# Optimization experiments

Hardware: AMD Instinct MI355X
Metric: run time of the kernel (lower is better)

Reference implementation:

```python
import jax, jax.numpy as jnp
import numpy as np

NUM_HEADS = 16

def setup_inputs() -> dict:
    key = jax.random.key(0)
    ks = jax.random.split(key, 5)
    N, T, D = 16, 4096, 1024
    # Linear weights stored as (in, out): y = x @ W + b (equivalent to torch x @ W.T + b)
    return {
        "x": jax.random.normal(ks[0], (N, T, D), jnp.float32),
        "w_qkv": jax.random.normal(ks[1], (D, 3 * D), jnp.float32) * (D ** -0.5),
        "b_qkv": jax.random.normal(ks[2], (3 * D,), jnp.float32) * 0.02,
        "w_proj": jax.random.normal(ks[3], (D, D), jnp.float32) * (D ** -0.5),
        "b_proj": jax.random.normal(ks[4], (D,), jnp.float32) * 0.02,
    }

def reference(x, w_qkv, b_qkv, w_proj, b_proj):
    N, T, D = x.shape
    H = NUM_HEADS
    hd = D // H
    scale = hd ** -0.5
    qkv = x @ w_qkv + b_qkv                      # (N,T,3D)
    qkv = qkv.reshape(N, T, 3, H, hd)
    q, k, v = qkv[:, :, 0], qkv[:, :, 1], qkv[:, :, 2]   # each (N,T,H,hd)
    # Faithful to source: matmul over last two dims -> scores across HEADS, (N,T,H,H)
    attn = jnp.einsum('nthd,ntgd->nthg', q * scale, k)
    attn = jax.nn.softmax(attn, axis=-1)
    out = jnp.einsum('nthg,ntgd->nthd', attn, v)         # (N,T,H,hd)
    # Faithful: transpose(2,1) then flatten -> (N,H,T,hd).reshape(N,T,D)
    out = out.transpose(0, 2, 1, 3).reshape(N, T, D)
    return out @ w_proj + b_proj
```

## Files before the change

kernel.cpp:

```cpp
#include <hip/hip_runtime.h>
#include <hip/hip_bf16.h>
#include <stdint.h>

typedef __bf16 bf16x8 __attribute__((ext_vector_type(8)));
typedef float f32x4 __attribute__((ext_vector_type(4)));
typedef unsigned short us8 __attribute__((ext_vector_type(8)));

__device__ __forceinline__ float bf2f(unsigned short u) {
    return __uint_as_float(((unsigned)u) << 16);
}
__device__ __forceinline__ unsigned short f2bf(float f) {
    __bf16 b = (__bf16)f;
    return __builtin_bit_cast(unsigned short, b);
}

__device__ __forceinline__ void gload16(const char* g, char* l) {
    __builtin_amdgcn_global_load_lds(
        (const __attribute__((address_space(1))) void*)g,
        (__attribute__((address_space(3))) void*)l, 16, 0, 0);
}

__global__ __launch_bounds__(256) void transpose_cast(
    const float* __restrict__ in, unsigned short* __restrict__ out,
    int K, int N)
{
    __shared__ float tile[32][33];
    const int tx = threadIdx.x, ty = threadIdx.y;
    const int n0 = blockIdx.x * 32, k0 = blockIdx.y * 32;
    #pragma unroll
    for (int i = 0; i < 32; i += 8)
        tile[ty + i][tx] = in[(long)(k0 + ty + i) * N + n0 + tx];
    __syncthreads();
    #pragma unroll
    for (int i = 0; i < 32; i += 8)
        out[(long)(n0 + ty + i) * K + k0 + tx] = f2bf(tile[tx][ty + i]);
}

__global__ __launch_bounds__(256) void cast_f32_bf16(
    const float* __restrict__ in, unsigned short* __restrict__ out, long n)
{
    const long stride = (long)gridDim.x * 256 * 8;
    for (long i = ((long)blockIdx.x * 256 + threadIdx.x) * 8; i < n; i += stride) {
        const f32x4 u0 = *(const f32x4*)&in[i];
        const f32x4 u1 = *(const f32x4*)&in[i + 4];
        us8 w;
        #pragma unroll
        for (int e = 0; e < 4; ++e) { w[e] = f2bf(u0[e]); w[e + 4] = f2bf(u1[e]); }
        *(us8*)&out[i] = w;
    }
}

#define MFMA16x16(a, b, c) __builtin_amdgcn_mfma_f32_16x16x32_bf16(a, b, c, 0, 0, 0)

template<bool OUT_BF16>
__global__ __launch_bounds__(512, 2)
void gemm256(const unsigned short* __restrict__ A,
             const unsigned short* __restrict__ BT,
             const float* __restrict__ bias,
             void* __restrict__ Cp,
             int M, int N, int K)
{
    extern __shared__ char smem[];
    const int tid  = threadIdx.x;
    const int lane = tid & 63;
    const int w    = tid >> 6;
    const int wm   = w >> 2;
    const int wn   = w & 3;

    const int nwg  = gridDim.x;
    const int bid0 = blockIdx.x;
    const int bid  = (bid0 & 7) * (nwg >> 3) + (bid0 >> 3);
    const int nbx  = N >> 8;
    const int bx   = bid % nbx, by = bid / nbx;
    const long rowStart = (long)by * 256;
    const int  colStart = bx * 256;

    const int  KT = K >> 6;
    const long Kb = (long)K * 2;

    const int srow = w * 8 + (lane >> 3);
    const int scol = ((lane & 7) ^ (lane >> 3)) << 4;
    const char* aStage = (const char*)A  + (rowStart + srow) * Kb + scol;
    const char* bStage = (const char*)BT + ((long)colStart + srow) * Kb + scol;
    const int ldsW = w * 1024;

    const int fr = lane & 15;
    const int kq = lane >> 4;
    const int kswz0 = (kq * 16)      ^ ((fr & 7) << 4);
    const int kswz1 = (64 + kq * 16) ^ ((fr & 7) << 4);
    const int aRowBase = (wm * 128 + fr) * 128;
    const int bRowBase = (wn * 64 + fr) * 128 + 32768;

    f32x4 acc[8][4] = {};

    #pragma unroll
    for (int tt = 0; tt < 2; ++tt) {
        #pragma unroll
        for (int j = 0; j < 4; ++j)
            gload16(aStage + (long)j * 64 * Kb + (long)tt * 128,
                    smem + tt * 65536 + j * 8192 + ldsW);
        #pragma unroll
        for (int j = 0; j < 4; ++j)
            gload16(bStage + (long)j * 64 * Kb + (long)tt * 128,
                    smem + tt * 65536 + 32768 + j * 8192 + ldsW);
    }

    #pragma unroll 2
    for (int t = 0; t < KT; ++t) {
        const int bufOff = (t & 1) * 65536;
        if (t < KT - 1) asm volatile("s_waitcnt vmcnt(8)");
        else            asm volatile("s_waitcnt vmcnt(0)");
        __builtin_amdgcn_s_barrier();
        __builtin_amdgcn_sched_barrier(0);

        bf16x8 a0[4][2], b01[2][2];
        #pragma unroll
        for (int mi = 0; mi < 4; ++mi) {
            a0[mi][0] = *(const bf16x8*)(smem + bufOff + aRowBase + mi * 2048 + kswz0);
            a0[mi][1] = *(const bf16x8*)(smem + bufOff + aRowBase + mi * 2048 + kswz1);
        }
        #pragma unroll
        for (int ni = 0; ni < 2; ++ni) {
            b01[ni][0] = *(const bf16x8*)(smem + bufOff + bRowBase + ni * 2048 + kswz0);
            b01[ni][1] = *(const bf16x8*)(smem + bufOff + bRowBase + ni * 2048 + kswz1);
        }
        __builtin_amdgcn_s_setprio(1);
        #pragma unroll
        for (int mi = 0; mi < 4; ++mi)
            #pragma unroll
            for (int ni = 0; ni < 2; ++ni) {
                acc[mi][ni] = MFMA16x16(a0[mi][0], b01[ni][0], acc[mi][ni]);
                acc[mi][ni] = MFMA16x16(a0[mi][1], b01[ni][1], acc[mi][ni]);
            }
        __builtin_amdgcn_s_setprio(0);
        __builtin_amdgcn_s_barrier();
        __builtin_amdgcn_sched_barrier(0);

        bf16x8 b23[2][2];
        #pragma unroll
        for (int nj = 0; nj < 2; ++nj) {
            b23[nj][0] = *(const bf16x8*)(smem + bufOff + bRowBase + (2 + nj) * 2048 + kswz0);
            b23[nj][1] = *(const bf16x8*)(smem + bufOff + bRowBase + (2 + nj) * 2048 + kswz1);
        }
        __builtin_amdgcn_s_setprio(1);
        #pragma unroll
        for (int mi = 0; mi < 4; ++mi)
            #pragma unroll
            for (int nj = 0; nj < 2; ++nj) {
                acc[mi][2 + nj] = MFMA16x16(a0[mi][0], b23[nj][0], acc[mi][2 + nj]);
                acc[mi][2 + nj] = MFMA16x16(a0[mi][1], b23[nj][1], acc[mi][2 + nj]);
            }
        __builtin_amdgcn_s_setprio(0);
        __builtin_amdgcn_s_barrier();
        __builtin_amdgcn_sched_barrier(0);
        if (t + 2 < KT) {
            gload16(aStage + (long)0 * 64 * Kb + (long)(t + 2) * 128,
                    smem + bufOff + 0 * 8192 + ldsW);
            gload16(aStage + (long)2 * 64 * Kb + (long)(t + 2) * 128,
                    smem + bufOff + 2 * 8192 + ldsW);
        }

        bf16x8 a4[4][2];
        #pragma unroll
        for (int mi = 0; mi < 4; ++mi) {
            a4[mi][0] = *(const bf16x8*)(smem + bufOff + aRowBase + (4 + mi) * 2048 + kswz0);
            a4[mi][1] = *(const bf16x8*)(smem + bufOff + aRowBase + (4 + mi) * 2048 + kswz1);
        }
        __builtin_amdgcn_s_setprio(1);
        #pragma unroll
        for (int mi = 0; mi < 4; ++mi)
            #pragma unroll
            for (int nj = 0; nj < 2; ++nj) {
                acc[4 + mi][2 + nj] = MFMA16x16(a4[mi][0], b23[nj][0], acc[4 + mi][2 + nj]);
                acc[4 + mi][2 + nj] = MFMA16x16(a4[mi][1], b23[nj][1], acc[4 + mi][2 + nj]);
            }
        __builtin_amdgcn_s_setprio(0);
        __builtin_amdgcn_s_barrier();
        __builtin_amdgcn_sched_barrier(0);
        if (t + 2 < KT) {
            #pragma unroll
            for (int j = 0; j < 4; ++j)
                gload16(bStage + (long)j * 64 * Kb + (long)(t + 2) * 128,
                        smem + bufOff + 32768 + j * 8192 + ldsW);
            gload16(aStage + (long)1 * 64 * Kb + (long)(t + 2) * 128,
                    smem + bufOff + 1 * 8192 + ldsW);
            gload16(aStage + (long)3 * 64 * Kb + (long)(t + 2) * 128,
                    smem + bufOff + 3 * 8192 + ldsW);
        }

        __builtin_amdgcn_s_setprio(1);
        #pragma unroll
        for (int mi = 0; mi < 4; ++mi)
            #pragma unroll
            for (int ni = 0; ni < 2; ++ni) {
                acc[4 + mi][ni] = MFMA16x16(a4[mi][0], b01[ni][0], acc[4 + mi][ni]);
                acc[4 + mi][ni] = MFMA16x16(a4[mi][1], b01[ni][1], acc[4 + mi][ni]);
            }
        __builtin_amdgcn_s_setprio(0);
        __builtin_amdgcn_sched_barrier(0);
    }

    float bv[4];
    #pragma unroll
    for (int ni = 0; ni < 4; ++ni)
        bv[ni] = bias[colStart + wn * 64 + ni * 16 + fr];
    #pragma unroll
    for (int mi = 0; mi < 8; ++mi) {
        #pragma unroll
        for (int ni = 0; ni < 4; ++ni) {
            const int col = colStart + wn * 64 + ni * 16 + fr;
            #pragma unroll
            for (int e = 0; e < 4; ++e) {
                const long row = rowStart + wm * 128 + mi * 16 + kq * 4 + e;
                const float val = acc[mi][ni][e] + bv[ni];
                if constexpr (OUT_BF16)
                    ((unsigned short*)Cp)[row * N + col] = f2bf(val);
                else
                    ((float*)Cp)[row * N + col] = val;
            }
        }
    }
}

__global__ __launch_bounds__(256) void attn_kernel(
    const unsigned short* __restrict__ qkv, unsigned short* __restrict__ out)
{
    __shared__ unsigned short qkvs[4][3072];
    __shared__ float ps[4][256];
    __shared__ unsigned short os[4][1024];
    const int tid = threadIdx.x, lane = tid & 63, wave = tid >> 6;
    const long blockTok = (long)blockIdx.x * 4;

    const unsigned short* src = qkv + blockTok * 3072;
    unsigned short* dstBase = &qkvs[0][0];
    #pragma unroll
    for (int i = 0; i < 6; ++i) {
        const int o = (i * 256 + tid) * 8;
        *(us8*)&dstBase[o] = *(const us8*)&src[o];
    }
    __syncthreads();

    const unsigned short* q = &qkvs[wave][0];
    const unsigned short* kk = &qkvs[wave][1024];
    const unsigned short* vv = &qkvs[wave][2048];
    const int h = lane >> 2, g4 = lane & 3;

    float s[4] = {0.f, 0.f, 0.f, 0.f};
    #pragma unroll
    for (int d0 = 0; d0 < 64; d0 += 8) {
        const us8 q8 = *(const us8*)&q[h * 64 + d0];
        float qf[8];
        #pragma unroll
        for (int e = 0; e < 8; ++e) qf[e] = bf2f(q8[e]);
        #pragma unroll
        for (int j = 0; j < 4; ++j) {
            const us8 k8 = *(const us8*)&kk[(g4 * 4 + j) * 64 + d0];
            #pragma unroll
            for (int e = 0; e < 8; ++e) s[j] += qf[e] * bf2f(k8[e]);
        }
    }
    #pragma unroll
    for (int j = 0; j < 4; ++j) s[j] *= 0.125f;

    float mx = fmaxf(fmaxf(s[0], s[1]), fmaxf(s[2], s[3]));
    mx = fmaxf(mx, __shfl_xor(mx, 1, 64));
    mx = fmaxf(mx, __shfl_xor(mx, 2, 64));
    float p[4], sum = 0.f;
    #pragma unroll
    for (int j = 0; j < 4; ++j) { p[j] = expf(s[j] - mx); sum += p[j]; }
    sum += __shfl_xor(sum, 1, 64);
    sum += __shfl_xor(sum, 2, 64);
    const float inv = 1.f / sum;
    #pragma unroll
    for (int j = 0; j < 4; ++j) ps[wave][h * 16 + g4 * 4 + j] = p[j] * inv;
    __syncthreads();

    const int db = lane & 3;
    float o16[16] = {};
    #pragma unroll
    for (int gq = 0; gq < 4; ++gq) {
        const f32x4 pv = *(const f32x4*)&ps[wave][h * 16 + gq * 4];
        #pragma unroll
        for (int j = 0; j < 4; ++j) {
            const float pg = pv[j];
            const int g = gq * 4 + j;
            const us8 v8a = *(const us8*)&vv[g * 64 + db * 16];
            const us8 v8b = *(const us8*)&vv[g * 64 + db * 16 + 8];
            #pragma unroll
            for (int e = 0; e < 8; ++e) {
                o16[e]     += pg * bf2f(v8a[e]);
                o16[8 + e] += pg * bf2f(v8b[e]);
            }
        }
    }
    us8 w0, w1;
    #pragma unroll
    for (int e = 0; e < 8; ++e) { w0[e] = f2bf(o16[e]); w1[e] = f2bf(o16[8 + e]); }
    *(us8*)&os[wave][h * 64 + db * 16] = w0;
    *(us8*)&os[wave][h * 64 + db * 16 + 8] = w1;
    __syncthreads();

    #pragma unroll
    for (int i = 0; i < 2; ++i) {
        const int c = i * 256 + tid;
        const int w2 = c >> 7;
        const int cc = c & 127;
        const long m = blockTok + w2;
        const long n_ = m >> 12;
        const int t = (int)(m & 4095);
        const int hh = cc >> 3, slot = cc & 7;
        const long row = n_ * 4096 + hh * 256 + (t >> 4);
        const long colb = (long)(t & 15) * 128 + slot * 16;
        *(us8*)((char*)out + row * 2048 + colb) = *(const us8*)&os[w2][cc * 8];
    }
}

extern "C" void kernel_launch(void* const* d_in, const int* in_sizes, int n_in,
                              void* d_out, int out_size, void* d_ws, size_t ws_size,
                              hipStream_t stream) {
    const float* x      = (const float*)d_in[0];
    const float* w_qkv  = (const float*)d_in[1];
    const float* b_qkv  = (const float*)d_in[2];
    const float* w_proj = (const float*)d_in[3];
    const float* b_proj = (const float*)d_in[4];

    const long M = 65536;
    const size_t QKV_B = (size_t)M * 3072 * 2;
    const size_t XB_B  = (size_t)M * 1024 * 2;
    const size_t WQ_B  = 3072 * 1024 * 2;
    const size_t WP_B  = 1024 * 1024 * 2;
    if (ws_size < QKV_B + XB_B + WQ_B + WP_B) return;

    char* ws = (char*)d_ws;
    unsigned short* qkv    = (unsigned short*)ws;
    unsigned short* xb     = (unsigned short*)(ws + QKV_B);
    unsigned short* wqkvT  = (unsigned short*)(ws + QKV_B + XB_B);
    unsigned short* wprojT = (unsigned short*)(ws + QKV_B + XB_B + WQ_B);

    hipFuncSetAttribute((const void*)gemm256<true>,
                        hipFuncAttributeMaxDynamicSharedMemorySize, 131072);
    hipFuncSetAttribute((const void*)gemm256<false>,
                        hipFuncAttributeMaxDynamicSharedMemorySize, 131072);

    dim3 tb(32, 8);
    transpose_cast<<<dim3(3072 / 32, 1024 / 32), tb, 0, stream>>>(w_qkv, wqkvT, 1024, 3072);
    transpose_cast<<<dim3(1024 / 32, 1024 / 32), tb, 0, stream>>>(w_proj, wprojT, 1024, 1024);
    cast_f32_bf16<<<2048, 256, 0, stream>>>(x, xb, M * 1024);

    gemm256<true><<<dim3((3072 / 256) * (M / 256)), 512, 131072, stream>>>(
        xb, wqkvT, b_qkv, qkv, (int)M, 3072, 1024);

    attn_kernel<<<dim3(M / 4), 256, 0, stream>>>(qkv, xb);

    gemm256<false><<<dim3((1024 / 256) * (M / 256)), 512, 131072, stream>>>(
        xb, wprojT, b_proj, d_out, (int)M, 1024, 1024);
}
```

Before: 791.5 us.

## Reorder GEMM main loop into four synchronized phases with manual double-buffer unroll

Rewrites the bf16 GEMM inner loop as a macro-expanded tile body, manually unrolled twice so each buffer offset is a compile-time constant. Each tile now runs four MFMA phases: A-low/B-low, A-high/B-low, A-low/B-high, A-high/B-high. Global-to-LDS prefetches are spread across the phase gaps, and the vmcnt wait moves to just before the last phase. Each phase gets an explicit lgkmcnt(0) wait and barriers. The aim is better overlap of LDS reads and global staging with MFMA work, at the cost of extra barriers and an implicit assumption that the number of K tiles is even.

Result: no change. 794.9 us (+0.4%).

```diff
diff --git a/kernel.cpp b/kernel.cpp
--- a/kernel.cpp
+++ b/kernel.cpp
@@ -51,6 +51,104 @@
 }
 
 #define MFMA16x16(a, b, c) __builtin_amdgcn_mfma_f32_16x16x32_bf16(a, b, c, 0, 0, 0)
+
+#define PHASE_SYNC_PRE()                          \
+    __builtin_amdgcn_sched_barrier(0);            \
+    __builtin_amdgcn_s_barrier();                 \
+    asm volatile("s_waitcnt lgkmcnt(0)");         \
+    __builtin_amdgcn_sched_barrier(0);            \
+    __builtin_amdgcn_s_setprio(1);
+
+#define PHASE_SYNC_POST()                         \
+    __builtin_amdgcn_s_setprio(0);                \
+    __builtin_amdgcn_sched_barrier(0);            \
+    __builtin_amdgcn_s_barrier();
+
+#define TILE_BODY(T, BUFOFF)                                                     \
+  do {                                                                           \
+    const bool doStage = ((T) + 2 < KT);                                         \
+    const long gk = (long)((T) + 2) * 128;                                       \
+    bf16x8 alo[4][2], ahi[4][2], blo[2][2], bhi[2][2];                           \
+                             \
+    _Pragma("unroll")                                                            \
+    for (int mi = 0; mi < 4; ++mi) {                                             \
+        alo[mi][0] = *(const bf16x8*)(smem + (BUFOFF) + aBase + mi*2048 + k0);   \
+        alo[mi][1] = *(const bf16x8*)(smem + (BUFOFF) + aBase + mi*2048 + k1);   \
+    }                                                                            \
+    _Pragma("unroll")                                                            \
+    for (int ni = 0; ni < 2; ++ni) {                                             \
+        blo[ni][0] = *(const bf16x8*)(smem + (BUFOFF) + bBase + ni*2048 + k0);   \
+        blo[ni][1] = *(const bf16x8*)(smem + (BUFOFF) + bBase + ni*2048 + k1);   \
+    }                                                                            \
+    PHASE_SYNC_PRE()                                                             \
+    _Pragma("unroll")                                                            \
+    for (int mi = 0; mi < 4; ++mi)                                               \
+        _Pragma("unroll")                                                        \
+        for (int ni = 0; ni < 2; ++ni) {                                         \
+            acc[mi][ni] = MFMA16x16(alo[mi][0], blo[ni][0], acc[mi][ni]);        \
+            acc[mi][ni] = MFMA16x16(alo[mi][1], blo[ni][1], acc[mi][ni]);        \
+        }                                                                        \
+    PHASE_SYNC_POST()                                                            \
+                     \
+    _Pragma("unroll")                                                            \
+    for (int mi = 0; mi < 4; ++mi) {                                             \
+        ahi[mi][0] = *(const bf16x8*)(smem + (BUFOFF) + aBase + 8192 + mi*2048 + k0); \
+        ahi[mi][1] = *(const bf16x8*)(smem + (BUFOFF) + aBase + 8192 + mi*2048 + k1); \
+    }                                                                            \
+    if (doStage) {                                                               \
+        gload16(aStage + (long)(0*64)*Kb + gk, smem + (BUFOFF) + 0*8192 + ldsW); \
+        gload16(aStage + (long)(2*64)*Kb + gk, smem + (BUFOFF) + 2*8192 + ldsW); \
+    }                                                                            \
+    PHASE_SYNC_PRE()                                                             \
+    _Pragma("unroll")                                                            \
+    for (int mi = 0; mi < 4; ++mi)                                               \
+        _Pragma("unroll")                                                        \
+        for (int ni = 0; ni < 2; ++ni) {                                         \
+            acc[4+mi][ni] = MFMA16x16(ahi[mi][0], blo[ni][0], acc[4+mi][ni]);    \
+            acc[4+mi][ni] = MFMA16x16(ahi[mi][1], blo[ni][1], acc[4+mi][ni]);    \
+        }                                                                        \
+    PHASE_SYNC_POST()                                                            \
+                     \
+    _Pragma("unroll")                                                            \
+    for (int nj = 0; nj < 2; ++nj) {                                             \
+        bhi[nj][0] = *(const bf16x8*)(smem + (BUFOFF) + bBase + (2+nj)*2048 + k0); \
+        bhi[nj][1] = *(const bf16x8*)(smem + (BUFOFF) + bBase + (2+nj)*2048 + k1); \
+    }                                                                            \
+    if (doStage) {                                                               \
+        gload16(aStage + (long)(1*64)*Kb + gk, smem + (BUFOFF) + 1*8192 + ldsW); \
+        gload16(aStage + (long)(3*64)*Kb + gk, smem + (BUFOFF) + 3*8192 + ldsW); \
+    }                                                                            \
+    PHASE_SYNC_PRE()                                                             \
+    _Pragma("unroll")                                                            \
+    for (int mi = 0; mi < 4; ++mi)                                               \
+        _Pragma("unroll")                                                        \
+        for (int nj = 0; nj < 2; ++nj) {                                         \
+            acc[mi][2+nj] = MFMA16x16(alo[mi][0], bhi[nj][0], acc[mi][2+nj]);    \
+            acc[mi][2+nj] = MFMA16x16(alo[mi][1], bhi[nj][1], acc[mi][2+nj]);    \
+        }                                                                        \
+    PHASE_SYNC_POST()                                                            \
+                \
+    if (doStage) {                                                               \
+        _Pragma("unroll")                                                        \
+        for (int j = 0; j < 4; ++j)                                              \
+            gload16(bStage + (long)(j*64)*Kb + gk,                               \
+                    smem + (BUFOFF) + 32768 + j*8192 + ldsW);                    \
+    }                                                                            \
+    __builtin_amdgcn_sched_barrier(0);                                           \
+    if (doStage) asm volatile("s_waitcnt vmcnt(8)");                             \
+    else         asm volatile("s_waitcnt vmcnt(0)");                             \
+    __builtin_amdgcn_sched_barrier(0);                                           \
+    __builtin_amdgcn_s_barrier();                                                \
+    __builtin_amdgcn_s_setprio(1);                                               \
+    _Pragma("unroll")                                                            \
+    for (int mi = 0; mi < 4; ++mi)                                               \
+        _Pragma("unroll")                                                        \
+        for (int nj = 0; nj < 2; ++nj) {                                         \
+            acc[4+mi][2+nj] = MFMA16x16(ahi[mi][0], bhi[nj][0], acc[4+mi][2+nj]); \
+            acc[4+mi][2+nj] = MFMA16x16(ahi[mi][1], bhi[nj][1], acc[4+mi][2+nj]); \
+        }                                                                        \
+    PHASE_SYNC_POST()                                                            \
+  } while (0)
 
 template<bool OUT_BF16>
 __global__ __launch_bounds__(512, 2)
@@ -86,10 +184,11 @@
 
     const int fr = lane & 15;
     const int kq = lane >> 4;
-    const int kswz0 = (kq * 16)      ^ ((fr & 7) << 4);
-    const int kswz1 = (64 + kq * 16) ^ ((fr & 7) << 4);
-    const int aRowBase = (wm * 128 + fr) * 128;
-    const int bRowBase = (wn * 64 + fr) * 128 + 32768;
+    const int sw = (fr & 7) << 4;
+    const int k0 = (kq * 16) ^ sw;
+    const int k1 = (64 + kq * 16) ^ sw;
+    const int aBase = (wm * 128 + fr) * 128;
+    const int bBase = 32768 + (wn * 64 + fr) * 128;
 
     f32x4 acc[8][4] = {};
 
@@ -97,107 +196,20 @@
     for (int tt = 0; tt < 2; ++tt) {
         #pragma unroll
         for (int j = 0; j < 4; ++j)
-            gload16(aStage + (long)j * 64 * Kb + (long)tt * 128,
+            gload16(aStage + (long)(j * 64) * Kb + (long)tt * 128,
                     smem + tt * 65536 + j * 8192 + ldsW);
         #pragma unroll
         for (int j = 0; j < 4; ++j)
-            gload16(bStage + (long)j * 64 * Kb + (long)tt * 128,
+            gload16(bStage + (long)(j * 64) * Kb + (long)tt * 128,
                     smem + tt * 65536 + 32768 + j * 8192 + ldsW);
     }
-
-    #pragma unroll 2
-    for (int t = 0; t < KT; ++t) {
-        const int bufOff = (t & 1) * 65536;
-        if (t < KT - 1) asm volatile("s_waitcnt vmcnt(8)");
-        else            asm volatile("s_waitcnt vmcnt(0)");
-        __builtin_amdgcn_s_barrier();
-        __builtin_amdgcn_sched_barrier(0);
-
-        bf16x8 a0[4][2], b01[2][2];
-        #pragma unroll
-        for (int mi = 0; mi < 4; ++mi) {
-            a0[mi][0] = *(const bf16x8*)(smem + bufOff + aRowBase + mi * 2048 + kswz0);
-            a0[mi][1] = *(const bf16x8*)(smem + bufOff + aRowBase + mi * 2048 + kswz1);
-        }
-        #pragma unroll
-        for (int ni = 0; ni < 2; ++ni) {
-            b01[ni][0] = *(const bf16x8*)(smem + bufOff + bRowBase + ni * 2048 + kswz0);
-            b01[ni][1] = *(const bf16x8*)(smem + bufOff + bRowBase + ni * 2048 + kswz1);
-        }
-        __builtin_amdgcn_s_setprio(1);
-        #pragma unroll
-        for (int mi = 0; mi < 4; ++mi)
-            #pragma unroll
-            for (int ni = 0; ni < 2; ++ni) {
-                acc[mi][ni] = MFMA16x16(a0[mi][0], b01[ni][0], acc[mi][ni]);
-                acc[mi][ni] = MFMA16x16(a0[mi][1], b01[ni][1], acc[mi][ni]);
-            }
-        __builtin_amdgcn_s_setprio(0);
-        __builtin_amdgcn_s_barrier();
-        __builtin_amdgcn_sched_barrier(0);
-
-        bf16x8 b23[2][2];
-        #pragma unroll
-        for (int nj = 0; nj < 2; ++nj) {
-            b23[nj][0] = *(const bf16x8*)(smem + bufOff + bRowBase + (2 + nj) * 2048 + kswz0);
-            b23[nj][1] = *(const bf16x8*)(smem + bufOff + bRowBase + (2 + nj) * 2048 + kswz1);
-        }
-        __builtin_amdgcn_s_setprio(1);
-        #pragma unroll
-        for (int mi = 0; mi < 4; ++mi)
-            #pragma unroll
-            for (int nj = 0; nj < 2; ++nj) {
-                acc[mi][2 + nj] = MFMA16x16(a0[mi][0], b23[nj][0], acc[mi][2 + nj]);
-                acc[mi][2 + nj] = MFMA16x16(a0[mi][1], b23[nj][1], acc[mi][2 + nj]);
-            }
-        __builtin_amdgcn_s_setprio(0);
-        __builtin_amdgcn_s_barrier();
-        __builtin_amdgcn_sched_barrier(0);
-        if (t + 2 < KT) {
-            gload16(aStage + (long)0 * 64 * Kb + (long)(t + 2) * 128,
-                    smem + bufOff + 0 * 8192 + ldsW);
-            gload16(aStage + (long)2 * 64 * Kb + (long)(t + 2) * 128,
-                    smem + bufOff + 2 * 8192 + ldsW);
-        }
-
-        bf16x8 a4[4][2];
-        #pragma unroll
-        for (int mi = 0; mi < 4; ++mi) {
-            a4[mi][0] = *(const bf16x8*)(smem + bufOff + aRowBase + (4 + mi) * 2048 + kswz0);
-            a4[mi][1] = *(const bf16x8*)(smem + bufOff + aRowBase + (4 + mi) * 2048 + kswz1);
-        }
-        __builtin_amdgcn_s_setprio(1);
-        #pragma unroll
-        for (int mi = 0; mi < 4; ++mi)
-            #pragma unroll
-            for (int nj = 0; nj < 2; ++nj) {
-                acc[4 + mi][2 + nj] = MFMA16x16(a4[mi][0], b23[nj][0], acc[4 + mi][2 + nj]);
-                acc[4 + mi][2 + nj] = MFMA16x16(a4[mi][1], b23[nj][1], acc[4 + mi][2 + nj]);
-            }
-        __builtin_amdgcn_s_setprio(0);
-        __builtin_amdgcn_s_barrier();
-        __builtin_amdgcn_sched_barrier(0);
-        if (t + 2 < KT) {
-            #pragma unroll
-            for (int j = 0; j < 4; ++j)
-                gload16(bStage + (long)j * 64 * Kb + (long)(t + 2) * 128,
-                        smem + bufOff + 32768 + j * 8192 + ldsW);
-            gload16(aStage + (long)1 * 64 * Kb + (long)(t + 2) * 128,
-                    smem + bufOff + 1 * 8192 + ldsW);
-            gload16(aStage + (long)3 * 64 * Kb + (long)(t + 2) * 128,
-                    smem + bufOff + 3 * 8192 + ldsW);
-        }
-
-        __builtin_amdgcn_s_setprio(1);
-        #pragma unroll
-        for (int mi = 0; mi < 4; ++mi)
-            #pragma unroll
-            for (int ni = 0; ni < 2; ++ni) {
-                acc[4 + mi][ni] = MFMA16x16(a4[mi][0], b01[ni][0], acc[4 + mi][ni]);
-                acc[4 + mi][ni] = MFMA16x16(a4[mi][1], b01[ni][1], acc[4 + mi][ni]);
-            }
-        __builtin_amdgcn_s_setprio(0);
-        __builtin_amdgcn_sched_barrier(0);
+    asm volatile("s_waitcnt vmcnt(8)");
+    __builtin_amdgcn_s_barrier();
+
+    #pragma unroll 1
+    for (int tp = 0; tp < KT / 2; ++tp) {
+        TILE_BODY(2 * tp,     0);
+        TILE_BODY(2 * tp + 1, 65536);
     }
 
     float bv[4];
```
